# Optimization experiments

Measured on AMD Instinct MI355X. Metric: run time of the kernel, lower is better.

Reference implementation:

```python
import jax, jax.numpy as jnp
import numpy as np

# MLA config (must match init_kwargs)
D_MODEL = 2048
NUM_HEADS = 16
HEAD_DIM = D_MODEL // NUM_HEADS          # 128
D_LATENT = 512
D_QK = D_LATENT // 2                      # 256
D_V = D_LATENT - D_QK                     # 256
ROPE_DIM = 64
QK_DEC = HEAD_DIM - ROPE_DIM              # 64
B, S = 2, 2048


def _glorot(key, shape):
    lim = np.sqrt(6.0 / (shape[0] + shape[1]))
    return jax.random.uniform(key, shape, jnp.float32, -lim, lim)


def setup_inputs() -> dict:
    key = jax.random.key(0)
    ks = jax.random.split(key, 8)
    return {
        "x": jax.random.normal(ks[0], (B, S, D_MODEL), jnp.float32),
        "W_comp": _glorot(ks[1], (D_MODEL, D_LATENT)),
        "W_q_dec": _glorot(ks[2], (D_QK, NUM_HEADS * QK_DEC)),
        "W_k_dec": _glorot(ks[3], (D_QK, NUM_HEADS * QK_DEC)),
        "W_v_dec": _glorot(ks[4], (D_V, NUM_HEADS * HEAD_DIM)),
        "W_rope_q": _glorot(ks[5], (D_MODEL, NUM_HEADS * ROPE_DIM)),
        "W_rope_k": _glorot(ks[6], (D_MODEL, NUM_HEADS * ROPE_DIM)),
        "W_out": _glorot(ks[7], (D_MODEL, D_MODEL)),
    }


def _apply_rope(t):
    # t: [B, S, H, ROPE_DIM]; rotate-half formulation with base 10000
    half = ROPE_DIM // 2
    inv_freq = 1.0 / (10000.0 ** (jnp.arange(0, ROPE_DIM, 2, dtype=jnp.float32) / ROPE_DIM))
    ang = jnp.arange(t.shape[1], dtype=jnp.float32)[:, None] * inv_freq[None, :]  # [S, half]
    cos = jnp.cos(ang)[None, :, None, :]
    sin = jnp.sin(ang)[None, :, None, :]
    t1, t2 = t[..., :half], t[..., half:]
    return jnp.concatenate([t1 * cos - t2 * sin, t1 * sin + t2 * cos], axis=-1)


def reference(x, W_comp, W_q_dec, W_k_dec, W_v_dec, W_rope_q, W_rope_k, W_out):
    # Compress to shared latent [B,S,d_latent]
    compressed = jnp.einsum("bsd,dl->bsl", x, W_comp)
    c_qk = compressed[:, :, :D_QK]
    c_v = compressed[:, :, D_QK:]

    # Decompress content parts and project RoPE parts from raw input
    q_no_rope = jnp.einsum("bsl,lh->bsh", c_qk, W_q_dec)   # [B,S,H*QK_DEC]
    k_no_rope = jnp.einsum("bsl,lh->bsh", c_qk, W_k_dec)
    v = jnp.einsum("bsl,lh->bsh", c_v, W_v_dec).reshape(B, S, NUM_HEADS, HEAD_DIM)
    q_rope = jnp.einsum("bsd,dh->bsh", x, W_rope_q)        # [B,S,H*ROPE_DIM]
    k_rope = jnp.einsum("bsd,dh->bsh", x, W_rope_k)

    # Faithful to source: concat along flat feature dim, then reshape to heads
    q = jnp.concatenate([q_no_rope, q_rope], axis=-1).reshape(B, S, NUM_HEADS, HEAD_DIM)
    k = jnp.concatenate([k_no_rope, k_rope], axis=-1).reshape(B, S, NUM_HEADS, HEAD_DIM)

    # Apply RoPE to last ROPE_DIM dims of each head
    q = jnp.concatenate([q[..., :QK_DEC], _apply_rope(q[..., QK_DEC:])], axis=-1)
    k = jnp.concatenate([k[..., :QK_DEC], _apply_rope(k[..., QK_DEC:])], axis=-1)

    scale = 1.0 / jnp.sqrt(jnp.float32(HEAD_DIM))
    scores = jnp.einsum("bqhd,bkhd->bhqk", q, k) * scale   # [B,H,S,S]
    attn = jax.nn.softmax(scores, axis=-1)
    ctx = jnp.einsum("bhqk,bkhd->bqhd", attn, v).reshape(B, S, D_MODEL)
    return jnp.einsum("bsd,de->bse", ctx, W_out)
```

## Files before the change

### kernel.cpp

```cpp
#include <hip/hip_runtime.h>
#include <stdint.h>

typedef __bf16 bf16x8 __attribute__((ext_vector_type(8)));
typedef __bf16 bf16x4 __attribute__((ext_vector_type(4)));
typedef float f32x4 __attribute__((ext_vector_type(4)));
typedef float f32x16 __attribute__((ext_vector_type(16)));

constexpr int NB   = 2;
constexpr int SEQ  = 2048;
constexpr int DM   = 2048;
constexpr int NH   = 16;
constexpr int HD   = 128;
constexpr int DL   = 512;
constexpr int ROWS = NB * SEQ;

__device__ __forceinline__ void gload16(const void* g, void* l) {
  __builtin_amdgcn_global_load_lds((const __attribute__((address_space(1))) uint32_t*)(const void*)g,
                                   (__attribute__((address_space(3))) uint32_t*)(void*)l, 16, 0, 0);
}

__device__ __forceinline__ uint32_t pk2(float lo, float hi) {
  union { __bf16 h[2]; uint32_t u; } x;
  x.h[0] = (__bf16)lo; x.h[1] = (__bf16)hi;
  return x.u;
}

__global__ __launch_bounds__(256) void cast_bf16(const float* __restrict__ in,
                                                 __bf16* __restrict__ out, int n4) {
  int i = blockIdx.x * blockDim.x + threadIdx.x;
  int stride = gridDim.x * blockDim.x;
  for (int k = i; k < n4; k += stride) {
    float4 v = ((const float4*)in)[k];
    union { __bf16 h[4]; uint2 u; } uo;
    uo.h[0] = (__bf16)v.x; uo.h[1] = (__bf16)v.y;
    uo.h[2] = (__bf16)v.z; uo.h[3] = (__bf16)v.w;
    ((uint2*)out)[k] = uo.u;
  }
}

__global__ __launch_bounds__(256) void transpose_cast(const float* __restrict__ in,
                                                      __bf16* __restrict__ out,
                                                      int R, int C) {
  __shared__ float t[32][33];
  int r0 = blockIdx.y * 32, c0 = blockIdx.x * 32;
  int tx = threadIdx.x, ty = threadIdx.y;
#pragma unroll
  for (int i = 0; i < 4; ++i)
    t[ty + 8*i][tx] = in[(size_t)(r0 + ty + 8*i) * C + c0 + tx];
  __syncthreads();
#pragma unroll
  for (int i = 0; i < 4; ++i)
    out[(size_t)(c0 + ty + 8*i) * R + r0 + tx] = (__bf16)t[tx][ty + 8*i];
}

__global__ __launch_bounds__(256) void transpose_v(const __bf16* __restrict__ v,
                                                   __bf16* __restrict__ vt) {
  __shared__ __bf16 t[32][33];
  int b = blockIdx.z >> 4, h = blockIdx.z & 15;
  int s0 = blockIdx.x * 32, d0 = blockIdx.y * 32;
  int tx = threadIdx.x, ty = threadIdx.y;
#pragma unroll
  for (int i = 0; i < 4; ++i)
    t[ty + 8*i][tx] = v[(size_t)(b*SEQ + s0 + ty + 8*i) * 2048 + h*128 + d0 + tx];
  __syncthreads();
#pragma unroll
  for (int i = 0; i < 4; ++i)
    vt[((size_t)(b*NH + h) * 128 + d0 + ty + 8*i) * 2048 + s0 + tx] = t[tx][ty + 8*i];
}

template <typename CT>
__global__ __launch_bounds__(256) void gemm_bt(const __bf16* __restrict__ A, int lda,
                                               const __bf16* __restrict__ Bt, int ldb,
                                               CT* __restrict__ C, int ldc, int K_) {
  __shared__ __align__(16) char As[16384];
  __shared__ __align__(16) char Bs[16384];
  const int m0 = blockIdx.y * 128, n0 = blockIdx.x * 128;
  const int t = threadIdx.x;
  const int wid = t >> 6, lane = t & 63;
  const int wr = (wid >> 1) * 64, wc = (wid & 1) * 64;
  const int lr = lane & 15, lg = lane >> 4;
  f32x4 acc[4][4] = {};
  for (int k0 = 0; k0 < K_; k0 += 64) {
    __syncthreads();
#pragma unroll
    for (int i = 0; i < 4; ++i) {
      int obi = wid * 4096 + i * 1024;
      int o   = obi + lane * 16;
      int row = o >> 7, sb = o & 127;
      int cb  = sb ^ ((row & 7) << 4);
      gload16((const char*)A  + ((size_t)(m0 + row) * lda + k0) * 2 + cb, As + obi);
      gload16((const char*)Bt + ((size_t)(n0 + row) * ldb + k0) * 2 + cb, Bs + obi);
    }
    __syncthreads();
#pragma unroll
    for (int kk = 0; kk < 2; ++kk) {
      bf16x8 af[4], bfr[4];
#pragma unroll
      for (int mi = 0; mi < 4; ++mi) {
        int row = wr + mi*16 + lr;
        af[mi] = *(const bf16x8*)(As + row * 128 + ((kk*64 + 16*lg) ^ ((row & 7) << 4)));
      }
#pragma unroll
      for (int ni = 0; ni < 4; ++ni) {
        int row = wc + ni*16 + lr;
        bfr[ni] = *(const bf16x8*)(Bs + row * 128 + ((kk*64 + 16*lg) ^ ((row & 7) << 4)));
      }
#pragma unroll
      for (int mi = 0; mi < 4; ++mi)
#pragma unroll
        for (int ni = 0; ni < 4; ++ni)
          acc[mi][ni] = __builtin_amdgcn_mfma_f32_16x16x32_bf16(af[mi], bfr[ni], acc[mi][ni], 0, 0, 0);
    }
  }
#pragma unroll
  for (int mi = 0; mi < 4; ++mi)
#pragma unroll
    for (int ni = 0; ni < 4; ++ni) {
      int r = m0 + wr + mi*16 + lg*4;
      int c = n0 + wc + ni*16 + lr;
#pragma unroll
      for (int j = 0; j < 4; ++j)
        C[(size_t)(r + j) * ldc + c] = (CT)acc[mi][ni][j];
    }
}

__global__ __launch_bounds__(256) void rope_assemble(const __bf16* __restrict__ nr,
                                                     const __bf16* __restrict__ rp,
                                                     int ld, __bf16* __restrict__ full,
                                                     float SC) {
  __shared__ float cs[32], sn[32];
  const int bs = blockIdx.x;
  const int s = bs & (SEQ - 1);
  const int t = threadIdx.x;
  if (t < 32) {
    float inv = exp2f(-0.41524101186092029f * (float)t);
    float ang = (float)s * inv;
    sincosf(ang, &sn[t], &cs[t]);
  }
  __syncthreads();
  const __bf16* nrow = nr + (size_t)bs * ld;
  const __bf16* rrow = rp + (size_t)bs * ld;
  __bf16* orow = full + (size_t)bs * 2048;
  const int c0 = t * 8;
  const __bf16* src = (c0 < 1024) ? (nrow + c0) : (rrow + (c0 - 1024));
  const int dh = c0 & 127;
  bf16x8 v = *(const bf16x8*)src;
  bf16x8 o;
  if (dh < 64) {
#pragma unroll
    for (int i = 0; i < 8; ++i) o[i] = (__bf16)((float)v[i] * SC);
  } else if (dh < 96) {
    bf16x8 v2 = *(const bf16x8*)(src + 32);
#pragma unroll
    for (int i = 0; i < 8; ++i) {
      int j = dh - 64 + i;
      o[i] = (__bf16)(((float)v[i] * cs[j] - (float)v2[i] * sn[j]) * SC);
    }
  } else {
    bf16x8 v1 = *(const bf16x8*)(src - 32);
#pragma unroll
    for (int i = 0; i < 8; ++i) {
      int j = dh - 96 + i;
      o[i] = (__bf16)(((float)v1[i] * sn[j] + (float)v[i] * cs[j]) * SC);
    }
  }
  *(bf16x8*)(orow + c0) = o;
}

__global__ __launch_bounds__(256, 2) void attn_fwd(const __bf16* __restrict__ qf,
                                                   const __bf16* __restrict__ kf,
                                                   const __bf16* __restrict__ vt,
                                                   __bf16* __restrict__ ctx) {
  __shared__ __align__(16) char Ks[2][16384];
  __shared__ __align__(16) char Vs[2][16384];
  const int t = threadIdx.x;
  const int wid = t >> 6, lane = t & 63;
  const int lq = lane & 31, hi = lane >> 5;
  const int h = blockIdx.y, b = blockIdx.z;
  const int qrow = blockIdx.x * 128 + wid * 32 + lq;
  const char* kbh = (const char*)(kf + (size_t)b * SEQ * DM + h * HD);
  const char* vbh = (const char*)(vt + (size_t)(b * NH + h) * HD * SEQ);

  bf16x8 qfr[8];
  const __bf16* qrp = qf + (size_t)(b * SEQ + qrow) * DM + h * HD;
#pragma unroll
  for (int kk = 0; kk < 8; ++kk)
    qfr[kk] = *(const bf16x8*)(qrp + kk * 16 + 8 * hi);

  f32x16 accO[4] = {};
  float mrun = -1e30f, lsum = 0.f;

  auto stageK = [&](int buf, int kc) {
#pragma unroll
    for (int i = 0; i < 4; ++i) {
      int ob = wid * 4096 + i * 1024;
      int o  = ob + lane * 16;
      int key = o >> 8, sb = o & 255;
      int cb  = sb ^ ((key & 7) << 4);
      gload16(kbh + (size_t)(kc + key) * (DM * 2) + cb, Ks[buf] + ob);
    }
  };
  auto stageV = [&](int buf, int kc) {
#pragma unroll
    for (int i = 0; i < 4; ++i) {
      int ob = wid * 4096 + i * 1024;
      int o  = ob + lane * 16;
      int d = o >> 7, sb = o & 127;
      int cb = sb ^ ((d & 7) << 4);
      gload16(vbh + (size_t)d * (SEQ * 2) + (size_t)kc * 2 + cb, Vs[buf] + ob);
    }
  };

  stageK(0, 0); stageV(0, 0);
  __syncthreads();
  int cur = 0;
  for (int kc = 0; kc < SEQ; kc += 64) {
    if (kc + 64 < SEQ) { stageK(cur ^ 1, kc + 64); stageV(cur ^ 1, kc + 64); }

    f32x16 st[2] = {};
    __builtin_amdgcn_s_setprio(1);
#pragma unroll
    for (int tt = 0; tt < 2; ++tt) {
      const int key = tt * 32 + lq;
      const char* kb = Ks[cur] + key * 256;
      const int swz = (key & 7) << 4;
#pragma unroll
      for (int kk = 0; kk < 8; ++kk) {
        bf16x8 kfr = *(const bf16x8*)(kb + ((32 * kk + 16 * hi) ^ swz));
        st[tt] = __builtin_amdgcn_mfma_f32_32x32x16_bf16(kfr, qfr[kk], st[tt], 0, 0, 0);
      }
    }
    __builtin_amdgcn_s_setprio(0);

    float p[2][16];
    float cmax = -1e30f;
#pragma unroll
    for (int tt = 0; tt < 2; ++tt)
#pragma unroll
      for (int r = 0; r < 16; ++r) {
        p[tt][r] = st[tt][r];
        cmax = fmaxf(cmax, st[tt][r]);
      }
    cmax = fmaxf(cmax, __shfl_xor(cmax, 32));
    if (!__all(cmax - mrun <= 8.f)) {
      float mnew = fmaxf(mrun, cmax);
      float corr = __expf(mrun - mnew);
      lsum *= corr;
#pragma unroll
      for (int db = 0; db < 4; ++db) accO[db] *= corr;
      mrun = mnew;
    }
    float psum = 0.f;
#pragma unroll
    for (int tt = 0; tt < 2; ++tt)
#pragma unroll
      for (int r = 0; r < 16; ++r) {
        p[tt][r] = __expf(p[tt][r] - mrun);
        psum += p[tt][r];
      }
    psum += __shfl_xor(psum, 32);
    lsum += psum;

    bf16x8 pfrag[4];
#pragma unroll
    for (int sl = 0; sl < 4; ++sl) {
      const int tt = sl >> 1, kk = sl & 1;
      uint32_t a0 = pk2(p[tt][8*kk + 0], p[tt][8*kk + 1]);
      uint32_t a1 = pk2(p[tt][8*kk + 2], p[tt][8*kk + 3]);
      uint32_t b0 = pk2(p[tt][8*kk + 4], p[tt][8*kk + 5]);
      uint32_t b1 = pk2(p[tt][8*kk + 6], p[tt][8*kk + 7]);
      uint32_t pa0 = (uint32_t)__shfl_xor((int)a0, 32);
      uint32_t pa1 = (uint32_t)__shfl_xor((int)a1, 32);
      uint32_t pb0 = (uint32_t)__shfl_xor((int)b0, 32);
      uint32_t pb1 = (uint32_t)__shfl_xor((int)b1, 32);
      union { uint32_t u[4]; bf16x8 v; } pu;
      pu.u[0] = hi ? pb0 : a0;
      pu.u[1] = hi ? pb1 : a1;
      pu.u[2] = hi ? b0 : pa0;
      pu.u[3] = hi ? b1 : pa1;
      pfrag[sl] = pu.v;
    }

    __builtin_amdgcn_s_setprio(1);
#pragma unroll
    for (int db = 0; db < 4; ++db) {
      const int d = db * 32 + lq;
      const char* vb = Vs[cur] + d * 128;
      const int swz = (d & 7) << 4;
#pragma unroll
      for (int sl = 0; sl < 4; ++sl) {
        bf16x8 vfr = *(const bf16x8*)(vb + ((32 * sl + 16 * hi) ^ swz));
        accO[db] = __builtin_amdgcn_mfma_f32_32x32x16_bf16(vfr, pfrag[sl], accO[db], 0, 0, 0);
      }
    }
    __builtin_amdgcn_s_setprio(0);
    __syncthreads();
    cur ^= 1;
  }

  float inv = 1.f / lsum;
  __bf16* op = ctx + (size_t)(b * SEQ + qrow) * DM + h * HD;
#pragma unroll
  for (int db = 0; db < 4; ++db)
#pragma unroll
    for (int a = 0; a < 4; ++a) {
      bf16x4 o4;
#pragma unroll
      for (int j = 0; j < 4; ++j) o4[j] = (__bf16)(accO[db][4*a + j] * inv);
      *(bf16x4*)(op + db*32 + 8*a + 4*hi) = o4;
    }
}

extern "C" void kernel_launch(void* const* d_in, const int* in_sizes, int n_in,
                              void* d_out, int out_size, void* d_ws, size_t ws_size,
                              hipStream_t stream) {
  const float* x   = (const float*)d_in[0];
  const float* Wc  = (const float*)d_in[1];
  const float* Wq  = (const float*)d_in[2];
  const float* Wk  = (const float*)d_in[3];
  const float* Wv  = (const float*)d_in[4];
  const float* Wrq = (const float*)d_in[5];
  const float* Wrk = (const float*)d_in[6];
  const float* Wo  = (const float*)d_in[7];
  float* out = (float*)d_out;

  char* ws = (char*)d_ws;
  size_t off = 0;
  auto take = [&](size_t bytes) { char* p = ws + off; off += bytes; return (__bf16*)p; };
  __bf16* xb    = take((size_t)ROWS * DM * 2);
  __bf16* comp  = take((size_t)ROWS * DL * 2);
  __bf16* qnr   = take((size_t)ROWS * 1024 * 2);
  __bf16* knr   = take((size_t)ROWS * 1024 * 2);
  __bf16* qr    = take((size_t)ROWS * 1024 * 2);
  __bf16* kr    = take((size_t)ROWS * 1024 * 2);
  __bf16* vb    = take((size_t)ROWS * 2048 * 2);
  __bf16* qfull = take((size_t)ROWS * 2048 * 2);
  __bf16* kfull = take((size_t)ROWS * 2048 * 2);
  __bf16* WcT   = take((size_t)512 * 2048 * 2);
  __bf16* WqT   = take((size_t)1024 * 256 * 2);
  __bf16* WkT   = take((size_t)1024 * 256 * 2);
  __bf16* WvT   = take((size_t)2048 * 256 * 2);
  __bf16* WrqT  = take((size_t)1024 * 2048 * 2);
  __bf16* WrkT  = take((size_t)1024 * 2048 * 2);
  __bf16* WoT   = take((size_t)2048 * 2048 * 2);
  (void)knr; (void)kr; (void)WkT; (void)WrkT;
  __bf16* ctx = qnr;
  __bf16* vtr = qr;

  const float scale = 0.088388347648318447f;

  dim3 tb(32, 8);
  cast_bf16<<<4096, 256, 0, stream>>>(x, xb, ROWS * DM / 4);
  transpose_cast<<<dim3(512/32,  2048/32), tb, 0, stream>>>(Wc,  WcT,  2048, 512);
  transpose_cast<<<dim3(1024/32, 256/32),  tb, 0, stream>>>(Wq,  WqT,  256, 1024);
  transpose_cast<<<dim3(1024/32, 256/32),  tb, 0, stream>>>(Wk,  WkT,  256, 1024);
  transpose_cast<<<dim3(2048/32, 256/32),  tb, 0, stream>>>(Wv,  WvT,  256, 2048);
  transpose_cast<<<dim3(1024/32, 2048/32), tb, 0, stream>>>(Wrq, WrqT, 2048, 1024);
  transpose_cast<<<dim3(1024/32, 2048/32), tb, 0, stream>>>(Wrk, WrkT, 2048, 1024);
  transpose_cast<<<dim3(2048/32, 2048/32), tb, 0, stream>>>(Wo,  WoT,  2048, 2048);

  gemm_bt<__bf16><<<dim3(512/128, ROWS/128), 256, 0, stream>>>(xb, DM, WcT, DM, comp, DL, DM);
  gemm_bt<__bf16><<<dim3(2048/128, ROWS/128), 256, 0, stream>>>(xb, DM, WrqT, DM, qr, 2048, DM);
  gemm_bt<__bf16><<<dim3(2048/128, ROWS/128), 256, 0, stream>>>(comp, DL, WqT, 256, qnr, 2048, 256);
  gemm_bt<__bf16><<<dim3(2048/128, ROWS/128), 256, 0, stream>>>(comp + 256, DL, WvT, 256, vb, 2048, 256);

  rope_assemble<<<ROWS, 256, 0, stream>>>(qnr,        qr,        2048, qfull, scale);
  rope_assemble<<<ROWS, 256, 0, stream>>>(qnr + 1024, qr + 1024, 2048, kfull, 1.0f);
  transpose_v<<<dim3(SEQ/32, 128/32, NB*NH), tb, 0, stream>>>(vb, vtr);

  attn_fwd<<<dim3(SEQ/128, NH, NB), 256, 0, stream>>>(qfull, kfull, vtr, ctx);

  gemm_bt<float><<<dim3(2048/128, ROWS/128), 256, 0, stream>>>(ctx, DM, WoT, DM, out, 2048, DM);
}
```

Measured before the change: 403.6 us.

## Batch weight transposes and RoPE launches, stage GEMM epilogue through LDS

```diff
diff --git a/kernel.cpp b/kernel.cpp
--- a/kernel.cpp
+++ b/kernel.cpp
@@ -38,11 +38,19 @@
   }
 }
 
-__global__ __launch_bounds__(256) void transpose_cast(const float* __restrict__ in,
-                                                      __bf16* __restrict__ out,
-                                                      int R, int C) {
+struct TC7 {
+  const float* in[7];
+  __bf16* out[7];
+  int R[7], C[7];
+};
+__global__ __launch_bounds__(256) void transpose_cast7(TC7 d) {
+  const int z = blockIdx.z;
+  const int R = d.R[z], C = d.C[z];
+  const int r0 = blockIdx.y * 32, c0 = blockIdx.x * 32;
+  if (r0 >= R || c0 >= C) return;
   __shared__ float t[32][33];
-  int r0 = blockIdx.y * 32, c0 = blockIdx.x * 32;
+  const float* in = d.in[z];
+  __bf16* out = d.out[z];
   int tx = threadIdx.x, ty = threadIdx.y;
 #pragma unroll
   for (int i = 0; i < 4; ++i)
@@ -72,8 +80,9 @@
 __global__ __launch_bounds__(256) void gemm_bt(const __bf16* __restrict__ A, int lda,
                                                const __bf16* __restrict__ Bt, int ldb,
                                                CT* __restrict__ C, int ldc, int K_) {
-  __shared__ __align__(16) char As[16384];
-  __shared__ __align__(16) char Bs[16384];
+  __shared__ __align__(16) char smem[32768];
+  char* As = smem;
+  char* Bs = smem + 16384;
   const int m0 = blockIdx.y * 128, n0 = blockIdx.x * 128;
   const int t = threadIdx.x;
   const int wid = t >> 6, lane = t & 63;
@@ -112,24 +121,42 @@
           acc[mi][ni] = __builtin_amdgcn_mfma_f32_16x16x32_bf16(af[mi], bfr[ni], acc[mi][ni], 0, 0, 0);
     }
   }
-#pragma unroll
-  for (int mi = 0; mi < 4; ++mi)
-#pragma unroll
-    for (int ni = 0; ni < 4; ++ni) {
-      int r = m0 + wr + mi*16 + lg*4;
-      int c = n0 + wc + ni*16 + lr;
+  __syncthreads();
+  float* Lf = (float*)(smem + wid * 8192);
+#pragma unroll
+  for (int mi = 0; mi < 4; ++mi) {
+#pragma unroll
+    for (int ni = 0; ni < 4; ++ni)
 #pragma unroll
       for (int j = 0; j < 4; ++j)
-        C[(size_t)(r + j) * ldc + c] = (CT)acc[mi][ni][j];
-    }
-}
-
-__global__ __launch_bounds__(256) void rope_assemble(const __bf16* __restrict__ nr,
-                                                     const __bf16* __restrict__ rp,
-                                                     int ld, __bf16* __restrict__ full,
-                                                     float SC) {
+        Lf[(lg*4 + j) * 68 + ni*16 + lr] = acc[mi][ni][j];
+    CT* Cp = C + (size_t)(m0 + wr + mi*16 + lr) * ldc + n0 + wc + lg*16;
+    if constexpr (sizeof(CT) == 2) {
+      union { __bf16 h[8]; uint4 q; } o0, o1;
+#pragma unroll
+      for (int u = 0; u < 8; ++u) {
+        o0.h[u] = (__bf16)Lf[lr*68 + lg*16 + u];
+        o1.h[u] = (__bf16)Lf[lr*68 + lg*16 + 8 + u];
+      }
+      *(uint4*)(Cp)     = o0.q;
+      *(uint4*)(Cp + 8) = o1.q;
+    } else {
+#pragma unroll
+      for (int u = 0; u < 4; ++u)
+        *(f32x4*)(Cp + 4*u) = *(const f32x4*)&Lf[lr*68 + lg*16 + 4*u];
+    }
+    if (mi < 3) __syncthreads();
+  }
+}
+
+__global__ __launch_bounds__(256) void rope_assemble2(const __bf16* __restrict__ nr0,
+                                                      const __bf16* __restrict__ rp0,
+                                                      __bf16* __restrict__ qfull,
+                                                      __bf16* __restrict__ kfull,
+                                                      float qsc) {
   __shared__ float cs[32], sn[32];
   const int bs = blockIdx.x;
+  const int which = blockIdx.y;
   const int s = bs & (SEQ - 1);
   const int t = threadIdx.x;
   if (t < 32) {
@@ -138,9 +165,10 @@
     sincosf(ang, &sn[t], &cs[t]);
   }
   __syncthreads();
-  const __bf16* nrow = nr + (size_t)bs * ld;
-  const __bf16* rrow = rp + (size_t)bs * ld;
-  __bf16* orow = full + (size_t)bs * 2048;
+  const float SC = which ? 1.0f : qsc;
+  const __bf16* nrow = nr0 + which * 1024 + (size_t)bs * 2048;
+  const __bf16* rrow = rp0 + which * 1024 + (size_t)bs * 2048;
+  __bf16* orow = (which ? kfull : qfull) + (size_t)bs * 2048;
   const int c0 = t * 8;
   const __bf16* src = (c0 < 1024) ? (nrow + c0) : (rrow + (c0 - 1024));
   const int dh = c0 & 127;
@@ -343,7 +371,7 @@
   __bf16* WrqT  = take((size_t)1024 * 2048 * 2);
   __bf16* WrkT  = take((size_t)1024 * 2048 * 2);
   __bf16* WoT   = take((size_t)2048 * 2048 * 2);
-  (void)knr; (void)kr; (void)WkT; (void)WrkT;
+  (void)knr; (void)kr;
   __bf16* ctx = qnr;
   __bf16* vtr = qr;
 
@@ -351,21 +379,23 @@
 
   dim3 tb(32, 8);
   cast_bf16<<<4096, 256, 0, stream>>>(x, xb, ROWS * DM / 4);
-  transpose_cast<<<dim3(512/32,  2048/32), tb, 0, stream>>>(Wc,  WcT,  2048, 512);
-  transpose_cast<<<dim3(1024/32, 256/32),  tb, 0, stream>>>(Wq,  WqT,  256, 1024);
-  transpose_cast<<<dim3(1024/32, 256/32),  tb, 0, stream>>>(Wk,  WkT,  256, 1024);
-  transpose_cast<<<dim3(2048/32, 256/32),  tb, 0, stream>>>(Wv,  WvT,  256, 2048);
-  transpose_cast<<<dim3(1024/32, 2048/32), tb, 0, stream>>>(Wrq, WrqT, 2048, 1024);
-  transpose_cast<<<dim3(1024/32, 2048/32), tb, 0, stream>>>(Wrk, WrkT, 2048, 1024);
-  transpose_cast<<<dim3(2048/32, 2048/32), tb, 0, stream>>>(Wo,  WoT,  2048, 2048);
+
+  TC7 td;
+  td.in[0] = Wc;  td.out[0] = WcT;  td.R[0] = 2048; td.C[0] = 512;
+  td.in[1] = Wq;  td.out[1] = WqT;  td.R[1] = 256;  td.C[1] = 1024;
+  td.in[2] = Wk;  td.out[2] = WkT;  td.R[2] = 256;  td.C[2] = 1024;
+  td.in[3] = Wv;  td.out[3] = WvT;  td.R[3] = 256;  td.C[3] = 2048;
+  td.in[4] = Wrq; td.out[4] = WrqT; td.R[4] = 2048; td.C[4] = 1024;
+  td.in[5] = Wrk; td.out[5] = WrkT; td.R[5] = 2048; td.C[5] = 1024;
+  td.in[6] = Wo;  td.out[6] = WoT;  td.R[6] = 2048; td.C[6] = 2048;
+  transpose_cast7<<<dim3(64, 64, 7), tb, 0, stream>>>(td);
 
   gemm_bt<__bf16><<<dim3(512/128, ROWS/128), 256, 0, stream>>>(xb, DM, WcT, DM, comp, DL, DM);
   gemm_bt<__bf16><<<dim3(2048/128, ROWS/128), 256, 0, stream>>>(xb, DM, WrqT, DM, qr, 2048, DM);
   gemm_bt<__bf16><<<dim3(2048/128, ROWS/128), 256, 0, stream>>>(comp, DL, WqT, 256, qnr, 2048, 256);
   gemm_bt<__bf16><<<dim3(2048/128, ROWS/128), 256, 0, stream>>>(comp + 256, DL, WvT, 256, vb, 2048, 256);
 
-  rope_assemble<<<ROWS, 256, 0, stream>>>(qnr,        qr,        2048, qfull, scale);
-  rope_assemble<<<ROWS, 256, 0, stream>>>(qnr + 1024, qr + 1024, 2048, kfull, 1.0f);
+  rope_assemble2<<<dim3(ROWS, 2), 256, 0, stream>>>(qnr, qr, qfull, kfull, scale);
   transpose_v<<<dim3(SEQ/32, 128/32, NB*NH), tb, 0, stream>>>(vb, vtr);
 
   attn_fwd<<<dim3(SEQ/128, NH, NB), 256, 0, stream>>>(qfull, kfull, vtr, ctx);
```

New measurement: 400.8 us. About the same (-0.7%).
